# Kernel optimization log

Measured on AMD Instinct MI355X. Metric: run time of the kernel, lower is better.

The kernel has to match this reference:

```python
import jax, jax.numpy as jnp
import numpy as np

B, H, L, D = 1, 16, 4096, 64

def setup_inputs() -> dict:
    key = jax.random.key(0)
    kq, kk, kv = jax.random.split(key, 3)
    q = jax.random.normal(kq, (B, H, L, D), dtype=jnp.float32)
    k = jax.random.normal(kk, (B, H, L, D), dtype=jnp.float32)
    v = jax.random.normal(kv, (B, H, L, D), dtype=jnp.float32)
    return {"q": q, "k": k, "v": v}

def reference(q, k, v):
    d_tensor = q.shape[-1]
    # [B,H,L,L] score matrix (naive attention, as in the original module)
    score = jnp.einsum('bhqd,bhkd->bhqk', q, k) / jnp.sqrt(jnp.float32(d_tensor))
    score = jax.nn.softmax(score, axis=-1)
    out = jnp.einsum('bhqk,bhkd->bhqd', score, v)
    return (out, score)
```

## Files before the change

### kernel.cpp

```cpp
#include <hip/hip_runtime.h>

#define H_ 16
#define L_ 4096
#define D_ 64
#define S_ 72
#define NKT 64

typedef __attribute__((ext_vector_type(4))) float    f32x4;
typedef __attribute__((ext_vector_type(8))) short    s16x8;
typedef __attribute__((ext_vector_type(4))) short    s16x4;
typedef __attribute__((ext_vector_type(8))) _Float16 h16x8;
typedef __attribute__((ext_vector_type(4))) _Float16 h16x4;

__device__ __forceinline__ short f2bf(float x) {
    unsigned u = __float_as_uint(x);
    u = (u + 0x7fffu + ((u >> 16) & 1u)) >> 16;
    return (short)u;
}
__device__ __forceinline__ float bf2f(short b) {
    return __uint_as_float(((unsigned)(unsigned short)b) << 16);
}

__global__ __launch_bounds__(256) void vt_kernel(const float* __restrict__ v,
                                                 _Float16* __restrict__ vt) {
    __shared__ float tile[64][65];
    const int h = blockIdx.y, t = blockIdx.x, tid = threadIdx.x;
    const int c = tid & 15, r = tid >> 4;
    const float* src = v + ((size_t)(h * L_ + t * 64)) * D_;
    for (int i = 0; i < 4; ++i) {
        int n = r + 16 * i;
        f32x4 x = *(const f32x4*)(src + (size_t)n * D_ + c * 4);
        tile[n][c * 4 + 0] = x.x;
        tile[n][c * 4 + 1] = x.y;
        tile[n][c * 4 + 2] = x.z;
        tile[n][c * 4 + 3] = x.w;
    }
    __syncthreads();
    _Float16* dst = vt + (size_t)h * D_ * L_ + t * 64;
    for (int j = 0; j < 4; ++j) {
        int d = r + 16 * j;
        int n0 = c * 4;
        h16x4 y;
        y.x = (_Float16)tile[n0 + 0][d];
        y.y = (_Float16)tile[n0 + 1][d];
        y.z = (_Float16)tile[n0 + 2][d];
        y.w = (_Float16)tile[n0 + 3][d];
        *(h16x4*)(dst + (size_t)d * L_ + n0) = y;
    }
}

__device__ __forceinline__ void stage_split(const float* __restrict__ src,
                                            short* __restrict__ hiB,
                                            short* __restrict__ loB,
                                            int tid, float scale) {
    const int c = (tid & 15) * 4, r0 = tid >> 4;
    for (int i = 0; i < 4; ++i) {
        int r = r0 + 16 * i;
        f32x4 x = *(const f32x4*)(src + (size_t)r * D_ + c);
        x.x *= scale; x.y *= scale; x.z *= scale; x.w *= scale;
        s16x4 hi, lo;
        short h0 = f2bf(x.x); hi.x = h0; lo.x = f2bf(x.x - bf2f(h0));
        short h1 = f2bf(x.y); hi.y = h1; lo.y = f2bf(x.y - bf2f(h1));
        short h2 = f2bf(x.z); hi.z = h2; lo.z = f2bf(x.z - bf2f(h2));
        short h3 = f2bf(x.w); hi.w = h3; lo.w = f2bf(x.w - bf2f(h3));
        *(s16x4*)(hiB + r * S_ + c) = hi;
        *(s16x4*)(loB + r * S_ + c) = lo;
    }
}

__global__ __launch_bounds__(256, 2) void attn_kernel(
    const float* __restrict__ q, const float* __restrict__ k,
    const _Float16* __restrict__ vt,
    float* __restrict__ out, float* __restrict__ score)
{
    __shared__ __align__(16) short    Qh[64 * S_], Ql[64 * S_], Kh[64 * S_], Kl[64 * S_];
    __shared__ __align__(16) _Float16 Ps[64 * S_], Vs[64 * S_];
    __shared__ float redM[4][64], redL[4][64];

    const int h = blockIdx.y, qb = blockIdx.x, tid = threadIdx.x;
    const int w = tid >> 6, lane = tid & 63, lrow = lane & 15, lgrp = lane >> 4;

    stage_split(q + ((size_t)(h * L_ + qb * 64)) * D_, Qh, Ql, tid, 0.125f);
    __syncthreads();

    s16x8 bQh[4][2], bQl[4][2];
    for (int mt = 0; mt < 4; ++mt)
        for (int ks = 0; ks < 2; ++ks) {
            int off = (16 * mt + lrow) * S_ + lgrp * 8 + 32 * ks;
            bQh[mt][ks] = *(s16x8*)(Qh + off);
            bQl[mt][ks] = *(s16x8*)(Ql + off);
        }

    float M[4], Ls[4];
    for (int mt = 0; mt < 4; ++mt) { M[mt] = -1e30f; Ls[mt] = 0.f; }

    const float* kbase = k + (size_t)h * L_ * D_;

    for (int kt = 0; kt < NKT; ++kt) {
        __syncthreads();
        stage_split(kbase + (size_t)kt * 64 * D_, Kh, Kl, tid, 1.0f);
        __syncthreads();
        s16x8 aKh[2], aKl[2];
        for (int ks = 0; ks < 2; ++ks) {
            int off = (16 * w + lrow) * S_ + lgrp * 8 + 32 * ks;
            aKh[ks] = *(s16x8*)(Kh + off);
            aKl[ks] = *(s16x8*)(Kl + off);
        }
        for (int mt = 0; mt < 4; ++mt) {
            f32x4 acc = {0.f, 0.f, 0.f, 0.f};
            for (int ks = 0; ks < 2; ++ks) {
                acc = __builtin_amdgcn_mfma_f32_16x16x32_bf16(aKh[ks], bQh[mt][ks], acc, 0, 0, 0);
                acc = __builtin_amdgcn_mfma_f32_16x16x32_bf16(aKh[ks], bQl[mt][ks], acc, 0, 0, 0);
                acc = __builtin_amdgcn_mfma_f32_16x16x32_bf16(aKl[ks], bQh[mt][ks], acc, 0, 0, 0);
            }
            float tm = fmaxf(fmaxf(acc.x, acc.y), fmaxf(acc.z, acc.w));
            tm = fmaxf(tm, __shfl_xor(tm, 16));
            tm = fmaxf(tm, __shfl_xor(tm, 32));
            float nM = fmaxf(M[mt], tm);
            float s = __expf(acc.x - nM) + __expf(acc.y - nM)
                    + __expf(acc.z - nM) + __expf(acc.w - nM);
            s += __shfl_xor(s, 16);
            s += __shfl_xor(s, 32);
            Ls[mt] = Ls[mt] * __expf(M[mt] - nM) + s;
            M[mt] = nM;
        }
    }

    if (lgrp == 0)
        for (int mt = 0; mt < 4; ++mt) {
            redM[w][16 * mt + lrow] = M[mt];
            redL[w][16 * mt + lrow] = Ls[mt];
        }
    __syncthreads();
    float Mf[4], Li[4];
    for (int mt = 0; mt < 4; ++mt) {
        int m = 16 * mt + lrow;
        float m0 = redM[0][m], m1 = redM[1][m], m2 = redM[2][m], m3 = redM[3][m];
        float mm = fmaxf(fmaxf(m0, m1), fmaxf(m2, m3));
        float ls = redL[0][m] * __expf(m0 - mm) + redL[1][m] * __expf(m1 - mm)
                 + redL[2][m] * __expf(m2 - mm) + redL[3][m] * __expf(m3 - mm);
        Mf[mt] = mm; Li[mt] = 1.f / ls;
    }

    f32x4 accO[4];
    for (int dt = 0; dt < 4; ++dt) accO[dt] = (f32x4){0.f, 0.f, 0.f, 0.f};

    float* scbase = score + ((size_t)(h * L_ + qb * 64)) * L_;
    const _Float16* vtb = vt + (size_t)h * D_ * L_;

    for (int kt = 0; kt < NKT; ++kt) {
        __syncthreads();
        stage_split(kbase + (size_t)kt * 64 * D_, Kh, Kl, tid, 1.0f);
        {
            const int c8 = (tid & 7) * 8, r8 = tid >> 3;
            for (int i = 0; i < 2; ++i) {
                int d = r8 + 32 * i;
                h16x8 x = *(const h16x8*)(vtb + (size_t)d * L_ + kt * 64 + c8);
                *(h16x8*)(Vs + d * S_ + c8) = x;
            }
        }
        __syncthreads();
        s16x8 aKh[2], aKl[2];
        for (int ks = 0; ks < 2; ++ks) {
            int off = (16 * w + lrow) * S_ + lgrp * 8 + 32 * ks;
            aKh[ks] = *(s16x8*)(Kh + off);
            aKl[ks] = *(s16x8*)(Kl + off);
        }
        for (int mt = 0; mt < 4; ++mt) {
            f32x4 acc = {0.f, 0.f, 0.f, 0.f};
            for (int ks = 0; ks < 2; ++ks) {
                acc = __builtin_amdgcn_mfma_f32_16x16x32_bf16(aKh[ks], bQh[mt][ks], acc, 0, 0, 0);
                acc = __builtin_amdgcn_mfma_f32_16x16x32_bf16(aKh[ks], bQl[mt][ks], acc, 0, 0, 0);
                acc = __builtin_amdgcn_mfma_f32_16x16x32_bf16(aKl[ks], bQh[mt][ks], acc, 0, 0, 0);
            }
            int m = 16 * mt + lrow;
            f32x4 p;
            p.x = __expf(acc.x - Mf[mt]) * Li[mt];
            p.y = __expf(acc.y - Mf[mt]) * Li[mt];
            p.z = __expf(acc.z - Mf[mt]) * Li[mt];
            p.w = __expf(acc.w - Mf[mt]) * Li[mt];
            *(f32x4*)(scbase + (size_t)m * L_ + kt * 64 + 16 * w + lgrp * 4) = p;
            h16x4 ph;
            ph.x = (_Float16)p.x; ph.y = (_Float16)p.y;
            ph.z = (_Float16)p.z; ph.w = (_Float16)p.w;
            *(h16x4*)(Ps + m * S_ + 16 * w + lgrp * 4) = ph;
        }
        __syncthreads();
        for (int ks = 0; ks < 2; ++ks) {
            s16x8 aPs = *(s16x8*)((short*)Ps + (16 * w + lrow) * S_ + lgrp * 8 + 32 * ks);
            h16x8 aP = __builtin_bit_cast(h16x8, aPs);
            for (int dt = 0; dt < 4; ++dt) {
                h16x8 bV = *(h16x8*)(Vs + (16 * dt + lrow) * S_ + lgrp * 8 + 32 * ks);
                accO[dt] = __builtin_amdgcn_mfma_f32_16x16x32_f16(aP, bV, accO[dt], 0, 0, 0);
            }
        }
    }

    float* obase = out + ((size_t)(h * L_ + qb * 64)) * D_;
    for (int dt = 0; dt < 4; ++dt)
        for (int r2 = 0; r2 < 4; ++r2) {
            int m = 16 * w + lgrp * 4 + r2;
            obase[(size_t)m * D_ + 16 * dt + lrow] = accO[dt][r2];
        }
}

extern "C" void kernel_launch(void* const* d_in, const int* in_sizes, int n_in,
                              void* d_out, int out_size, void* d_ws, size_t ws_size,
                              hipStream_t stream) {
    const float* q = (const float*)d_in[0];
    const float* kk = (const float*)d_in[1];
    const float* v = (const float*)d_in[2];
    float* out = (float*)d_out;
    float* score = out + (size_t)H_ * L_ * D_;
    _Float16* vt = (_Float16*)d_ws;

    vt_kernel<<<dim3(L_ / 64, H_), 256, 0, stream>>>(v, vt);
    attn_kernel<<<dim3(L_ / 64, H_), 256, 0, stream>>>(q, kk, vt, out, score);
}
```

Measured before the change: 1.580 ms.

## Pre-split K and V into MFMA fragment layout, drop LDS staging in attention loop

Adds prepass kernels that convert K to hi/lo bf16 and V to fp16, stored directly in per-lane MFMA fragment order. The attention kernel then loads fragments straight from global memory with register double-buffering, removing the per-tile LDS staging, the bf16 splitting and the per-tile __syncthreads. The PV product now uses 16x16x16 MFMA fed from the P accumulator registers, so P no longer goes through LDS. Each wave therefore holds a partial output for all 64 rows, and these are summed across waves in LDS at the end. Blocks are also swizzled across heads. The cost is more accumulator registers, an extra prepass kernel and a serialized cross-wave reduction at the end.

```diff
diff --git a/kernel.cpp b/kernel.cpp
--- a/kernel.cpp
+++ b/kernel.cpp
@@ -3,14 +3,12 @@
 #define H_ 16
 #define L_ 4096
 #define D_ 64
-#define S_ 72
 #define NKT 64
 
 typedef __attribute__((ext_vector_type(4))) float    f32x4;
 typedef __attribute__((ext_vector_type(8))) short    s16x8;
-typedef __attribute__((ext_vector_type(4))) short    s16x4;
+typedef __attribute__((ext_vector_type(4))) _Float16 h16x4;
 typedef __attribute__((ext_vector_type(8))) _Float16 h16x8;
-typedef __attribute__((ext_vector_type(4))) _Float16 h16x4;
 
 __device__ __forceinline__ short f2bf(float x) {
     unsigned u = __float_as_uint(x);
@@ -21,199 +19,288 @@
     return __uint_as_float(((unsigned)(unsigned short)b) << 16);
 }
 
-__global__ __launch_bounds__(256) void vt_kernel(const float* __restrict__ v,
-                                                 _Float16* __restrict__ vt) {
+__global__ __launch_bounds__(256) void kfrag_kernel(const float* __restrict__ k,
+                                                    short* __restrict__ khi,
+                                                    short* __restrict__ klo) {
     __shared__ float tile[64][65];
-    const int h = blockIdx.y, t = blockIdx.x, tid = threadIdx.x;
-    const int c = tid & 15, r = tid >> 4;
-    const float* src = v + ((size_t)(h * L_ + t * 64)) * D_;
-    for (int i = 0; i < 4; ++i) {
-        int n = r + 16 * i;
-        f32x4 x = *(const f32x4*)(src + (size_t)n * D_ + c * 4);
-        tile[n][c * 4 + 0] = x.x;
-        tile[n][c * 4 + 1] = x.y;
-        tile[n][c * 4 + 2] = x.z;
-        tile[n][c * 4 + 3] = x.w;
+    const int h = blockIdx.y, kt = blockIdx.x, tid = threadIdx.x;
+    {
+        const int c = tid & 15, r = tid >> 4;
+        const float* src = k + ((size_t)(h * L_ + kt * 64)) * D_;
+        for (int i = 0; i < 4; ++i) {
+            int n = r + 16 * i;
+            f32x4 x = *(const f32x4*)(src + (size_t)n * D_ + c * 4);
+            tile[n][c * 4 + 0] = x.x;
+            tile[n][c * 4 + 1] = x.y;
+            tile[n][c * 4 + 2] = x.z;
+            tile[n][c * 4 + 3] = x.w;
+        }
     }
     __syncthreads();
-    _Float16* dst = vt + (size_t)h * D_ * L_ + t * 64;
-    for (int j = 0; j < 4; ++j) {
-        int d = r + 16 * j;
-        int n0 = c * 4;
-        h16x4 y;
-        y.x = (_Float16)tile[n0 + 0][d];
-        y.y = (_Float16)tile[n0 + 1][d];
-        y.z = (_Float16)tile[n0 + 2][d];
-        y.w = (_Float16)tile[n0 + 3][d];
-        *(h16x4*)(dst + (size_t)d * L_ + n0) = y;
-    }
-}
-
-__device__ __forceinline__ void stage_split(const float* __restrict__ src,
-                                            short* __restrict__ hiB,
-                                            short* __restrict__ loB,
-                                            int tid, float scale) {
-    const int c = (tid & 15) * 4, r0 = tid >> 4;
-    for (int i = 0; i < 4; ++i) {
-        int r = r0 + 16 * i;
-        f32x4 x = *(const f32x4*)(src + (size_t)r * D_ + c);
-        x.x *= scale; x.y *= scale; x.z *= scale; x.w *= scale;
-        s16x4 hi, lo;
-        short h0 = f2bf(x.x); hi.x = h0; lo.x = f2bf(x.x - bf2f(h0));
-        short h1 = f2bf(x.y); hi.y = h1; lo.y = f2bf(x.y - bf2f(h1));
-        short h2 = f2bf(x.z); hi.z = h2; lo.z = f2bf(x.z - bf2f(h2));
-        short h3 = f2bf(x.w); hi.w = h3; lo.w = f2bf(x.w - bf2f(h3));
-        *(s16x4*)(hiB + r * S_ + c) = hi;
-        *(s16x4*)(loB + r * S_ + c) = lo;
-    }
-}
+    const size_t base = (size_t)(h * NKT + kt) * (8 * 64 * 8);
+    for (int e = 0; e < 2; ++e) {
+        int idx = tid + 256 * e;
+        int l = idx & 63, set = idx >> 6;
+        int row = 16 * (set >> 1) + (l & 15);
+        int col = 32 * (set & 1) + 8 * (l >> 4);
+        s16x8 hi, lo;
+        #pragma unroll
+        for (int j = 0; j < 8; ++j) {
+            float x = tile[row][col + j];
+            short hb = f2bf(x);
+            hi[j] = hb;
+            lo[j] = f2bf(x - bf2f(hb));
+        }
+        *(s16x8*)(khi + base + (size_t)idx * 8) = hi;
+        *(s16x8*)(klo + base + (size_t)idx * 8) = lo;
+    }
+}
+
+__global__ __launch_bounds__(256) void vfrag_kernel(const float* __restrict__ v,
+                                                    _Float16* __restrict__ vf) {
+    __shared__ float tile[64][65];
+    const int h = blockIdx.y, kt = blockIdx.x, tid = threadIdx.x;
+    {
+        const int c = tid & 15, r = tid >> 4;
+        const float* src = v + ((size_t)(h * L_ + kt * 64)) * D_;
+        for (int i = 0; i < 4; ++i) {
+            int n = r + 16 * i;
+            f32x4 x = *(const f32x4*)(src + (size_t)n * D_ + c * 4);
+            tile[n][c * 4 + 0] = x.x;
+            tile[n][c * 4 + 1] = x.y;
+            tile[n][c * 4 + 2] = x.z;
+            tile[n][c * 4 + 3] = x.w;
+        }
+    }
+    __syncthreads();
+    const size_t base = (size_t)(h * NKT + kt) * (8 * 64 * 8);
+    for (int e = 0; e < 2; ++e) {
+        int idx = tid + 256 * e;
+        int l = idx & 63, set = idx >> 6;
+        int s = set >> 1, p = set & 1;
+        int g = l >> 4, r = l & 15;
+        h16x8 y;
+        #pragma unroll
+        for (int j = 0; j < 4; ++j) {
+            y[j]     = (_Float16)tile[16 * s + 4 * g + j][32 * p + r];
+            y[4 + j] = (_Float16)tile[16 * s + 4 * g + j][32 * p + 16 + r];
+        }
+        *(h16x8*)(vf + base + (size_t)idx * 8) = y;
+    }
+}
+
+#define KFO(kt_, ks_) (((size_t)(((kt_) * 8 + w * 2 + (ks_)) * 64 + lane)) * 8)
 
 __global__ __launch_bounds__(256, 2) void attn_kernel(
-    const float* __restrict__ q, const float* __restrict__ k,
-    const _Float16* __restrict__ vt,
+    const float* __restrict__ q,
+    const short* __restrict__ khi, const short* __restrict__ klo,
+    const _Float16* __restrict__ vf,
     float* __restrict__ out, float* __restrict__ score)
 {
-    __shared__ __align__(16) short    Qh[64 * S_], Ql[64 * S_], Kh[64 * S_], Kl[64 * S_];
-    __shared__ __align__(16) _Float16 Ps[64 * S_], Vs[64 * S_];
-    __shared__ float redM[4][64], redL[4][64];
-
-    const int h = blockIdx.y, qb = blockIdx.x, tid = threadIdx.x;
-    const int w = tid >> 6, lane = tid & 63, lrow = lane & 15, lgrp = lane >> 4;
-
-    stage_split(q + ((size_t)(h * L_ + qb * 64)) * D_, Qh, Ql, tid, 0.125f);
-    __syncthreads();
+    __shared__ float Ored[64][65];
+    __shared__ float redM[4][4][16], redL[4][4][16];
+
+    int flat = blockIdx.y * gridDim.x + blockIdx.x;
+    flat = (flat & 7) * 128 + (flat >> 3);
+    const int h = flat >> 6, qb = flat & 63;
+
+    const int tid = threadIdx.x, w = tid >> 6;
+    const int lane = tid & 63, lrow = lane & 15, lgrp = lane >> 4;
 
     s16x8 bQh[4][2], bQl[4][2];
+    const float* qbase = q + ((size_t)(h * L_ + qb * 64)) * D_;
+    #pragma unroll
     for (int mt = 0; mt < 4; ++mt)
+        #pragma unroll
         for (int ks = 0; ks < 2; ++ks) {
-            int off = (16 * mt + lrow) * S_ + lgrp * 8 + 32 * ks;
-            bQh[mt][ks] = *(s16x8*)(Qh + off);
-            bQl[mt][ks] = *(s16x8*)(Ql + off);
-        }
+            const float* p0 = qbase + (size_t)(16 * mt + lrow) * D_ + 32 * ks + 8 * lgrp;
+            f32x4 a = *(const f32x4*)p0;
+            f32x4 b = *(const f32x4*)(p0 + 4);
+            float xs[8] = {a.x, a.y, a.z, a.w, b.x, b.y, b.z, b.w};
+            s16x8 hi, lo;
+            #pragma unroll
+            for (int j = 0; j < 8; ++j) {
+                float x = xs[j] * 0.125f;
+                short hb = f2bf(x);
+                hi[j] = hb;
+                lo[j] = f2bf(x - bf2f(hb));
+            }
+            bQh[mt][ks] = hi;
+            bQl[mt][ks] = lo;
+        }
+
+    const size_t hoff = (size_t)h * (L_ * D_);
+    const short*    khs = khi + hoff;
+    const short*    kls = klo + hoff;
+    const _Float16* vfs = vf + hoff;
 
     float M[4], Ls[4];
+    #pragma unroll
     for (int mt = 0; mt < 4; ++mt) { M[mt] = -1e30f; Ls[mt] = 0.f; }
 
-    const float* kbase = k + (size_t)h * L_ * D_;
-
+    s16x8 kh[2], kl[2];
+    #pragma unroll
+    for (int ks = 0; ks < 2; ++ks) {
+        kh[ks] = *(const s16x8*)(khs + KFO(0, ks));
+        kl[ks] = *(const s16x8*)(kls + KFO(0, ks));
+    }
+    #pragma unroll 2
     for (int kt = 0; kt < NKT; ++kt) {
-        __syncthreads();
-        stage_split(kbase + (size_t)kt * 64 * D_, Kh, Kl, tid, 1.0f);
-        __syncthreads();
-        s16x8 aKh[2], aKl[2];
+        s16x8 nkh[2], nkl[2];
+        const int ktn = (kt + 1) & 63;
+        #pragma unroll
         for (int ks = 0; ks < 2; ++ks) {
-            int off = (16 * w + lrow) * S_ + lgrp * 8 + 32 * ks;
-            aKh[ks] = *(s16x8*)(Kh + off);
-            aKl[ks] = *(s16x8*)(Kl + off);
-        }
+            nkh[ks] = *(const s16x8*)(khs + KFO(ktn, ks));
+            nkl[ks] = *(const s16x8*)(kls + KFO(ktn, ks));
+        }
+        #pragma unroll
         for (int mt = 0; mt < 4; ++mt) {
             f32x4 acc = {0.f, 0.f, 0.f, 0.f};
+            #pragma unroll
             for (int ks = 0; ks < 2; ++ks) {
-                acc = __builtin_amdgcn_mfma_f32_16x16x32_bf16(aKh[ks], bQh[mt][ks], acc, 0, 0, 0);
-                acc = __builtin_amdgcn_mfma_f32_16x16x32_bf16(aKh[ks], bQl[mt][ks], acc, 0, 0, 0);
-                acc = __builtin_amdgcn_mfma_f32_16x16x32_bf16(aKl[ks], bQh[mt][ks], acc, 0, 0, 0);
+                acc = __builtin_amdgcn_mfma_f32_16x16x32_bf16(kh[ks], bQh[mt][ks], acc, 0, 0, 0);
+                acc = __builtin_amdgcn_mfma_f32_16x16x32_bf16(kh[ks], bQl[mt][ks], acc, 0, 0, 0);
+                acc = __builtin_amdgcn_mfma_f32_16x16x32_bf16(kl[ks], bQh[mt][ks], acc, 0, 0, 0);
             }
             float tm = fmaxf(fmaxf(acc.x, acc.y), fmaxf(acc.z, acc.w));
-            tm = fmaxf(tm, __shfl_xor(tm, 16));
-            tm = fmaxf(tm, __shfl_xor(tm, 32));
             float nM = fmaxf(M[mt], tm);
             float s = __expf(acc.x - nM) + __expf(acc.y - nM)
                     + __expf(acc.z - nM) + __expf(acc.w - nM);
-            s += __shfl_xor(s, 16);
-            s += __shfl_xor(s, 32);
             Ls[mt] = Ls[mt] * __expf(M[mt] - nM) + s;
             M[mt] = nM;
         }
-    }
-
-    if (lgrp == 0)
-        for (int mt = 0; mt < 4; ++mt) {
-            redM[w][16 * mt + lrow] = M[mt];
-            redL[w][16 * mt + lrow] = Ls[mt];
-        }
+        kh[0] = nkh[0]; kh[1] = nkh[1];
+        kl[0] = nkl[0]; kl[1] = nkl[1];
+    }
+
+    #pragma unroll
+    for (int mt = 0; mt < 4; ++mt) {
+        float m_ = M[mt], l_ = Ls[mt];
+        float mo = __shfl_xor(m_, 16), lo_ = __shfl_xor(l_, 16);
+        float mm = fmaxf(m_, mo);
+        l_ = l_ * __expf(m_ - mm) + lo_ * __expf(mo - mm);
+        m_ = mm;
+        mo = __shfl_xor(m_, 32); lo_ = __shfl_xor(l_, 32);
+        mm = fmaxf(m_, mo);
+        l_ = l_ * __expf(m_ - mm) + lo_ * __expf(mo - mm);
+        m_ = mm;
+        if (lgrp == 0) { redM[w][mt][lrow] = m_; redL[w][mt][lrow] = l_; }
+    }
     __syncthreads();
     float Mf[4], Li[4];
+    #pragma unroll
     for (int mt = 0; mt < 4; ++mt) {
-        int m = 16 * mt + lrow;
-        float m0 = redM[0][m], m1 = redM[1][m], m2 = redM[2][m], m3 = redM[3][m];
+        float m0 = redM[0][mt][lrow], m1 = redM[1][mt][lrow];
+        float m2 = redM[2][mt][lrow], m3 = redM[3][mt][lrow];
         float mm = fmaxf(fmaxf(m0, m1), fmaxf(m2, m3));
-        float ls = redL[0][m] * __expf(m0 - mm) + redL[1][m] * __expf(m1 - mm)
-                 + redL[2][m] * __expf(m2 - mm) + redL[3][m] * __expf(m3 - mm);
-        Mf[mt] = mm; Li[mt] = 1.f / ls;
-    }
-
-    f32x4 accO[4];
-    for (int dt = 0; dt < 4; ++dt) accO[dt] = (f32x4){0.f, 0.f, 0.f, 0.f};
+        float ls = redL[0][mt][lrow] * __expf(m0 - mm)
+                 + redL[1][mt][lrow] * __expf(m1 - mm)
+                 + redL[2][mt][lrow] * __expf(m2 - mm)
+                 + redL[3][mt][lrow] * __expf(m3 - mm);
+        Mf[mt] = mm;
+        Li[mt] = 1.f / ls;
+    }
+
+    f32x4 accO[4][4];
+    #pragma unroll
+    for (int mt = 0; mt < 4; ++mt)
+        #pragma unroll
+        for (int dt = 0; dt < 4; ++dt)
+            accO[mt][dt] = (f32x4){0.f, 0.f, 0.f, 0.f};
 
     float* scbase = score + ((size_t)(h * L_ + qb * 64)) * L_;
-    const _Float16* vtb = vt + (size_t)h * D_ * L_;
-
+
+    h16x8 vb[2];
+    #pragma unroll
+    for (int ks = 0; ks < 2; ++ks) {
+        kh[ks] = *(const s16x8*)(khs + KFO(0, ks));
+        kl[ks] = *(const s16x8*)(kls + KFO(0, ks));
+        vb[ks] = *(const h16x8*)(vfs + KFO(0, ks));
+    }
+    #pragma unroll 2
     for (int kt = 0; kt < NKT; ++kt) {
-        __syncthreads();
-        stage_split(kbase + (size_t)kt * 64 * D_, Kh, Kl, tid, 1.0f);
-        {
-            const int c8 = (tid & 7) * 8, r8 = tid >> 3;
-            for (int i = 0; i < 2; ++i) {
-                int d = r8 + 32 * i;
-                h16x8 x = *(const h16x8*)(vtb + (size_t)d * L_ + kt * 64 + c8);
-                *(h16x8*)(Vs + d * S_ + c8) = x;
-            }
-        }
-        __syncthreads();
-        s16x8 aKh[2], aKl[2];
+        s16x8 nkh[2], nkl[2];
+        h16x8 nvb[2];
+        const int ktn = (kt + 1) & 63;
+        #pragma unroll
         for (int ks = 0; ks < 2; ++ks) {
-            int off = (16 * w + lrow) * S_ + lgrp * 8 + 32 * ks;
-            aKh[ks] = *(s16x8*)(Kh + off);
-            aKl[ks] = *(s16x8*)(Kl + off);
-        }
+            nkh[ks] = *(const s16x8*)(khs + KFO(ktn, ks));
+            nkl[ks] = *(const s16x8*)(kls + KFO(ktn, ks));
+            nvb[ks] = *(const h16x8*)(vfs + KFO(ktn, ks));
+        }
+        h16x4 b0 = __builtin_shufflevector(vb[0], vb[0], 0, 1, 2, 3);
+        h16x4 b1 = __builtin_shufflevector(vb[0], vb[0], 4, 5, 6, 7);
+        h16x4 b2 = __builtin_shufflevector(vb[1], vb[1], 0, 1, 2, 3);
+        h16x4 b3 = __builtin_shufflevector(vb[1], vb[1], 4, 5, 6, 7);
+        #pragma unroll
         for (int mt = 0; mt < 4; ++mt) {
             f32x4 acc = {0.f, 0.f, 0.f, 0.f};
+            #pragma unroll
             for (int ks = 0; ks < 2; ++ks) {
-                acc = __builtin_amdgcn_mfma_f32_16x16x32_bf16(aKh[ks], bQh[mt][ks], acc, 0, 0, 0);
-                acc = __builtin_amdgcn_mfma_f32_16x16x32_bf16(aKh[ks], bQl[mt][ks], acc, 0, 0, 0);
-                acc = __builtin_amdgcn_mfma_f32_16x16x32_bf16(aKl[ks], bQh[mt][ks], acc, 0, 0, 0);
+                acc = __builtin_amdgcn_mfma_f32_16x16x32_bf16(kh[ks], bQh[mt][ks], acc, 0, 0, 0);
+                acc = __builtin_amdgcn_mfma_f32_16x16x32_bf16(kh[ks], bQl[mt][ks], acc, 0, 0, 0);
+                acc = __builtin_amdgcn_mfma_f32_16x16x32_bf16(kl[ks], bQh[mt][ks], acc, 0, 0, 0);
             }
-            int m = 16 * mt + lrow;
             f32x4 p;
             p.x = __expf(acc.x - Mf[mt]) * Li[mt];
             p.y = __expf(acc.y - Mf[mt]) * Li[mt];
             p.z = __expf(acc.z - Mf[mt]) * Li[mt];
             p.w = __expf(acc.w - Mf[mt]) * Li[mt];
-            *(f32x4*)(scbase + (size_t)m * L_ + kt * 64 + 16 * w + lgrp * 4) = p;
-            h16x4 ph;
-            ph.x = (_Float16)p.x; ph.y = (_Float16)p.y;
-            ph.z = (_Float16)p.z; ph.w = (_Float16)p.w;
-            *(h16x4*)(Ps + m * S_ + 16 * w + lgrp * 4) = ph;
+            *(f32x4*)(scbase + (size_t)(16 * mt + lrow) * L_ + kt * 64 + 16 * w + 4 * lgrp) = p;
+            h16x4 pa;
+            pa[0] = (_Float16)p.x; pa[1] = (_Float16)p.y;
+            pa[2] = (_Float16)p.z; pa[3] = (_Float16)p.w;
+            accO[mt][0] = __builtin_amdgcn_mfma_f32_16x16x16f16(pa, b0, accO[mt][0], 0, 0, 0);
+            accO[mt][1] = __builtin_amdgcn_mfma_f32_16x16x16f16(pa, b1, accO[mt][1], 0, 0, 0);
+            accO[mt][2] = __builtin_amdgcn_mfma_f32_16x16x16f16(pa, b2, accO[mt][2], 0, 0, 0);
+            accO[mt][3] = __builtin_amdgcn_mfma_f32_16x16x16f16(pa, b3, accO[mt][3], 0, 0, 0);
+        }
+        kh[0] = nkh[0]; kh[1] = nkh[1];
+        kl[0] = nkl[0]; kl[1] = nkl[1];
+        vb[0] = nvb[0]; vb[1] = nvb[1];
+    }
+
+    for (int w2 = 0; w2 < 4; ++w2) {
+        if (w == w2) {
+            #pragma unroll
+            for (int mt = 0; mt < 4; ++mt)
+                #pragma unroll
+                for (int dt = 0; dt < 4; ++dt) {
+                    int d = 16 * dt + lrow;
+                    #pragma unroll
+                    for (int r2 = 0; r2 < 4; ++r2) {
+                        int m = 16 * mt + 4 * lgrp + r2;
+                        if (w2 == 0) Ored[m][d] = accO[mt][dt][r2];
+                        else         Ored[m][d] += accO[mt][dt][r2];
+                    }
+                }
         }
         __syncthreads();
-        for (int ks = 0; ks < 2; ++ks) {
-            s16x8 aPs = *(s16x8*)((short*)Ps + (16 * w + lrow) * S_ + lgrp * 8 + 32 * ks);
-            h16x8 aP = __builtin_bit_cast(h16x8, aPs);
-            for (int dt = 0; dt < 4; ++dt) {
-                h16x8 bV = *(h16x8*)(Vs + (16 * dt + lrow) * S_ + lgrp * 8 + 32 * ks);
-                accO[dt] = __builtin_amdgcn_mfma_f32_16x16x32_f16(aP, bV, accO[dt], 0, 0, 0);
-            }
-        }
-    }
-
+    }
     float* obase = out + ((size_t)(h * L_ + qb * 64)) * D_;
-    for (int dt = 0; dt < 4; ++dt)
-        for (int r2 = 0; r2 < 4; ++r2) {
-            int m = 16 * w + lgrp * 4 + r2;
-            obase[(size_t)m * D_ + 16 * dt + lrow] = accO[dt][r2];
-        }
+    #pragma unroll
+    for (int i = 0; i < 4; ++i) {
+        int off = tid * 4 + 1024 * i;
+        int m = off >> 6, c = off & 63;
+        f32x4 x = {Ored[m][c], Ored[m][c + 1], Ored[m][c + 2], Ored[m][c + 3]};
+        *(f32x4*)(obase + off) = x;
+    }
 }
 
 extern "C" void kernel_launch(void* const* d_in, const int* in_sizes, int n_in,
                               void* d_out, int out_size, void* d_ws, size_t ws_size,
                               hipStream_t stream) {
     const float* q = (const float*)d_in[0];
-    const float* kk = (const float*)d_in[1];
+    const float* k = (const float*)d_in[1];
     const float* v = (const float*)d_in[2];
     float* out = (float*)d_out;
     float* score = out + (size_t)H_ * L_ * D_;
-    _Float16* vt = (_Float16*)d_ws;
-
-    vt_kernel<<<dim3(L_ / 64, H_), 256, 0, stream>>>(v, vt);
-    attn_kernel<<<dim3(L_ / 64, H_), 256, 0, stream>>>(q, kk, vt, out, score);
-}
+
+    short*    khi = (short*)d_ws;
+    short*    klo = (short*)((char*)d_ws + ((size_t)8 << 20));
+    _Float16* vfr = (_Float16*)((char*)d_ws + ((size_t)16 << 20));
+
+    kfrag_kernel<<<dim3(NKT, H_), 256, 0, stream>>>(k, khi, klo);
+    vfrag_kernel<<<dim3(NKT, H_), 256, 0, stream>>>(v, vfr);
+    attn_kernel<<<dim3(64, H_), 256, 0, stream>>>(q, khi, klo, vfr, out, score);
+}
```

Result: faster. 1.549 ms (-2.0%).
